# Optimization experiments

Measured on AMD Instinct MI355X. Metric: run time of the kernel, lower is better.

Reference implementation:

```python
import jax, jax.numpy as jnp
import numpy as np

B, NUM_PEAKS, PEAK_SIZE = 2, 64, 1000
MOTIF, HID, DEPTH, PROF_K = 640, 256, 7, 75


def conv1d(x, w, b, dilation=1):
    # x: (N, C, L), w: (O, I, K), valid padding
    out = jax.lax.conv_general_dilated(
        x, w, window_strides=(1,), padding='VALID',
        rhs_dilation=(dilation,), dimension_numbers=('NCH', 'OIH', 'NCH'))
    return out + b[None, :, None]


def setup_inputs() -> dict:
    key = jax.random.key(0)
    ks = jax.random.split(key, 10)
    L = NUM_PEAKS * PEAK_SIZE
    x = jax.random.normal(ks[0], (B, L, MOTIF), dtype=jnp.float32)
    peak_split = jnp.full((B * NUM_PEAKS,), PEAK_SIZE, dtype=jnp.int64) if jax.config.jax_enable_x64 else jnp.full((B * NUM_PEAKS,), PEAK_SIZE, dtype=jnp.int32)
    n_peaks = jnp.full((B,), NUM_PEAKS, dtype=jnp.int32)
    # parameters (kaiming-ish small init)
    w_proj = jax.random.normal(ks[1], (HID, MOTIF, 1), dtype=jnp.float32) / np.sqrt(MOTIF)
    b_proj = jnp.zeros((HID,), jnp.float32)
    w_dil = jax.random.normal(ks[2], (DEPTH, HID, HID, 3), dtype=jnp.float32) / np.sqrt(3 * HID)
    b_dil = jnp.zeros((DEPTH, HID), jnp.float32)
    w_prof = jax.random.normal(ks[3], (1, HID, PROF_K), dtype=jnp.float32) / np.sqrt(PROF_K * HID)
    b_prof = jnp.zeros((1,), jnp.float32)
    w_atpm = jax.random.normal(ks[4], (1, HID), dtype=jnp.float32) / np.sqrt(HID)
    b_atpm = jnp.zeros((1,), jnp.float32)
    return {
        'x': x, 'peak_split': peak_split, 'n_peaks': n_peaks, 'max_n_peaks': NUM_PEAKS,
        'w_proj': w_proj, 'b_proj': b_proj, 'w_dil': w_dil, 'b_dil': b_dil,
        'w_prof': w_prof, 'b_prof': b_prof, 'w_atpm': w_atpm, 'b_atpm': b_atpm,
    }


def reference(x, peak_split, n_peaks, max_n_peaks,
              w_proj, b_proj, w_dil, b_dil, w_prof, b_prof, w_atpm, b_atpm):
    # fast path: all samples have max_n_peaks uniform-size peaks
    batch, length, _ = x.shape
    num_peaks = int(np.asarray(n_peaks)[0])
    peak_size = length // num_peaks
    # 1x1 motif projection: (B, L, MOTIF) -> (B, HID, L)
    h = conv1d(jnp.transpose(x, (0, 2, 1)), w_proj, b_proj)
    # split into peaks: (B*num_peaks, HID, peak_size)
    h = jnp.transpose(h, (0, 2, 1)).reshape(batch * num_peaks, peak_size, HID)
    h = jnp.transpose(h, (0, 2, 1))
    # dilated conv tower with residual crop
    for i in range(DEPTH):
        dilation = 2 ** (i + 1)
        out = conv1d(h, w_dil[i], b_dil[i], dilation=dilation)
        crop = (h.shape[-1] - out.shape[-1]) // 2
        h = jax.nn.relu(out) + h[..., crop:-crop]
    peak_atpm = h.mean(axis=2)                      # (N, HID)
    peak_profile = conv1d(h, w_prof, b_prof)        # (N, 1, out_len)
    peak_atpm = jax.nn.softplus(peak_atpm @ w_atpm.T + b_atpm)
    peak_atpm = peak_atpm.reshape(batch, num_peaks, 1)
    peak_profile = jax.nn.softplus(peak_profile.reshape(batch, -1))
    return (peak_atpm, peak_profile)
```

## Files before the change

kernel.cpp:

```cpp
#include <hip/hip_runtime.h>
#include <hip/hip_bf16.h>
#include <math.h>

#define HID 256
#define MOTIF 640
#define PEAK 1000
#define NPEAKS 128
#define DEPTHN 7
#define PROFK 75
#define FINLEN 492
#define PROFLEN 418

typedef unsigned short u16;
typedef unsigned int u32;
typedef _Float16 f16x8 __attribute__((ext_vector_type(8)));
typedef float f32x16 __attribute__((ext_vector_type(16)));

__device__ __forceinline__ u16 f2h(float f) {
    _Float16 h = (_Float16)f; u16 b; __builtin_memcpy(&b, &h, 2); return b;
}
__device__ __forceinline__ float h2f(u16 b) {
    _Float16 h; __builtin_memcpy(&h, &b, 2); return (float)h;
}
__device__ __forceinline__ float hlo(u32 u) { return h2f((u16)(u & 0xffff)); }
__device__ __forceinline__ float hhi(u32 u) { return h2f((u16)(u >> 16)); }
__device__ __forceinline__ u32 pk2h(float a, float b) {
    return (u32)f2h(a) | ((u32)f2h(b) << 16);
}

__global__ __launch_bounds__(256) void conv_wdil1(const float* __restrict__ w,
                                                  u16* __restrict__ wf,
                                                  float* zp) {
    int i = blockIdx.x * 256 + threadIdx.x;
    if (zp && i < NPEAKS) zp[i] = 0.f;
    int cil = i & 15; int j = i >> 4;
    int c = j & 255; j >>= 8;
    int ci16 = j & 15; int k = j >> 4;
    wf[i] = f2h(w[((size_t)c * HID + ci16 * 16 + cil) * 3 + k]);
}

__global__ __launch_bounds__(256) void conv_wproj(const float* __restrict__ w,
                                                  u16* __restrict__ wf) {
    int i = blockIdx.x * 256 + threadIdx.x;
    if (i >= MOTIF * HID) return;
    int ml = i & 15;
    int c = (i >> 4) & 255;
    int m16 = i >> 12;
    wf[i] = f2h(w[(size_t)c * MOTIF + m16 * 16 + ml]);
}

template<int TAPS, int KCI, int DIL, bool SRCF32, bool RESID, bool ATPM>
__global__ __launch_bounds__(256, 3) void mfma_gemm(
    const void* __restrict__ src, int in_len, int in_stride,
    const u16* __restrict__ wf, const float* __restrict__ bias,
    u16* __restrict__ dst, int out_len,
    const float* __restrict__ watpm, float* part)
{
    constexpr int R = 128 + (TAPS - 1) * DIL;
    __shared__ __attribute__((aligned(16))) u16 Bs[8 * R * 8];
    __shared__ float aw[4];
    const int tid = threadIdx.x;
    const int wave = tid >> 6, lane = tid & 63;
    const int col = lane & 31, half = lane >> 5;
    const int cg = wave & 1, tg = wave >> 1;
    const int t0 = blockIdx.x * 128;
    const int c0 = blockIdx.y * 128;
    const int n  = blockIdx.z;

    const float* snf = (const float*)src + (size_t)n * in_len * in_stride;
    const u16*   snh = (const u16*)src + (size_t)n * in_len * in_stride;

    f32x16 acc[2][2];
    #pragma unroll
    for (int cs = 0; cs < 2; ++cs)
        #pragma unroll
        for (int ts = 0; ts < 2; ++ts)
            #pragma unroll
            for (int q = 0; q < 16; ++q) acc[cs][ts][q] = 0.f;

    for (int ci0 = 0; ci0 < KCI; ci0 += 64) {
        __syncthreads();
        for (int s = tid; s < R * 8; s += 256) {
            const int r = s >> 3, ch = s & 7;
            int g = t0 + r; if (g > in_len - 1) g = in_len - 1;
            u16* d = &Bs[(ch * R + r) * 8];
            if (SRCF32) {
                const float* p = snf + (size_t)g * in_stride + ci0 + ch * 8;
                float4 a = *(const float4*)p;
                float4 b = *(const float4*)(p + 4);
                uint4 o;
                o.x = pk2h(a.x, a.y); o.y = pk2h(a.z, a.w);
                o.z = pk2h(b.x, b.y); o.w = pk2h(b.z, b.w);
                *(uint4*)d = o;
            } else {
                *(uint4*)d = *(const uint4*)(snh + (size_t)g * in_stride + ci0 + ch * 8);
            }
        }
        __syncthreads();
        #pragma unroll
        for (int k = 0; k < TAPS; ++k) {
            #pragma unroll
            for (int s2 = 0; s2 < 4; ++s2) {
                const int ktile = k * (KCI / 16) + (ci0 >> 4) + s2;
                f16x8 bfv[2];
                #pragma unroll
                for (int ts = 0; ts < 2; ++ts)
                    bfv[ts] = *reinterpret_cast<const f16x8*>(
                        &Bs[((s2 * 2 + half) * R + tg * 64 + ts * 32 + col + k * DIL) * 8]);
                #pragma unroll
                for (int cs = 0; cs < 2; ++cs) {
                    const f16x8 af = *reinterpret_cast<const f16x8*>(
                        wf + ((size_t)(ktile * 256 + c0 + cg * 64 + cs * 32 + col) * 16 + half * 8));
                    acc[cs][0] = __builtin_amdgcn_mfma_f32_32x32x16_f16(af, bfv[0], acc[cs][0], 0, 0, 0);
                    acc[cs][1] = __builtin_amdgcn_mfma_f32_32x32x16_f16(af, bfv[1], acc[cs][1], 0, 0, 0);
                }
            }
        }
    }

    float apart = 0.f;
    #pragma unroll
    for (int ts = 0; ts < 2; ++ts) {
        const int t = t0 + tg * 64 + ts * 32 + col;
        if (t >= out_len) continue;
        const float* resf = snf + (size_t)(t + DIL) * in_stride;
        const u16*   resh = snh + (size_t)(t + DIL) * in_stride;
        u16* oh = dst + ((size_t)n * out_len + t) * HID;
        #pragma unroll
        for (int cs = 0; cs < 2; ++cs) {
            #pragma unroll
            for (int g = 0; g < 4; ++g) {
                const int c = c0 + cg * 64 + cs * 32 + g * 8 + half * 4;
                float4 bv = *(const float4*)(bias + c);
                float v0 = acc[cs][ts][g * 4 + 0] + bv.x;
                float v1 = acc[cs][ts][g * 4 + 1] + bv.y;
                float v2 = acc[cs][ts][g * 4 + 2] + bv.z;
                float v3 = acc[cs][ts][g * 4 + 3] + bv.w;
                if (RESID) {
                    if (SRCF32) {
                        float4 r = *(const float4*)(resf + c);
                        v0 = fmaxf(v0, 0.f) + r.x;
                        v1 = fmaxf(v1, 0.f) + r.y;
                        v2 = fmaxf(v2, 0.f) + r.z;
                        v3 = fmaxf(v3, 0.f) + r.w;
                    } else {
                        uint2 r = *(const uint2*)(resh + c);
                        v0 = fmaxf(v0, 0.f) + hlo(r.x);
                        v1 = fmaxf(v1, 0.f) + hhi(r.x);
                        v2 = fmaxf(v2, 0.f) + hlo(r.y);
                        v3 = fmaxf(v3, 0.f) + hhi(r.y);
                    }
                }
                if (ATPM) {
                    float4 wv = *(const float4*)(watpm + c);
                    apart += v0 * wv.x + v1 * wv.y + v2 * wv.z + v3 * wv.w;
                }
                uint2 o; o.x = pk2h(v0, v1); o.y = pk2h(v2, v3);
                *(uint2*)(oh + c) = o;
            }
        }
    }
    if (ATPM) {
        #pragma unroll
        for (int off = 32; off; off >>= 1) apart += __shfl_down(apart, off, 64);
        if (lane == 0) aw[wave] = apart;
        __syncthreads();
        if (tid == 0) atomicAdd(part + n, aw[0] + aw[1] + aw[2] + aw[3]);
    }
}

__global__ void atpm_fin(const float* __restrict__ part,
                         const float* __restrict__ batpm, float* __restrict__ out) {
    int i = threadIdx.x;
    float tot = part[i] / (float)FINLEN + batpm[0];
    out[i] = fmaxf(tot, 0.f) + log1pf(expf(-fabsf(tot)));
}

__global__ __launch_bounds__(256) void prof_kernel(
    const u16* __restrict__ h, const float* __restrict__ wprof,
    const float* __restrict__ bprof, float* __restrict__ out)
{
    __shared__ __attribute__((aligned(16))) float hs[64 * 204];
    __shared__ float red[128 * 8];
    const int tid = threadIdx.x;
    const int wave = tid >> 6, lane = tid & 63;
    const int ts = lane & 31, hw = lane >> 5;
    const int cig = wave * 2 + hw;
    const int n = blockIdx.y, t0 = blockIdx.x * 128;
    const u16* hn = h + (size_t)n * FINLEN * HID;
    float acc[4] = {0.f, 0.f, 0.f, 0.f};

    for (int ci0 = 0; ci0 < HID; ci0 += 64) {
        __syncthreads();
        {
            const int ci = tid & 63, rg = tid >> 6;
            for (int base = 0; base < 204; base += 16) {
                const int r0 = base + rg * 4;
                if (r0 >= 204) continue;
                float4 v;
                float* vp = (float*)&v;
                #pragma unroll
                for (int j = 0; j < 4; ++j) {
                    int g = t0 + r0 + j; if (g > FINLEN - 1) g = FINLEN - 1;
                    vp[j] = h2f(hn[(size_t)g * HID + ci0 + ci]);
                }
                *(float4*)&hs[ci * 204 + r0] = v;
            }
        }
        __syncthreads();
        for (int ci = 0; ci < 8; ++ci) {
            const int cia = cig * 8 + ci;
            const float4* hrow = (const float4*)&hs[cia * 204];
            const float* wrow = wprof + (size_t)(ci0 + cia) * PROFK;
            float wqf[84];
            #pragma unroll
            for (int q = 0; q < 3; ++q) wqf[q] = 0.f;
            #pragma unroll
            for (int q = 78; q < 84; ++q) wqf[q] = 0.f;
            #pragma unroll
            for (int k = 0; k < PROFK; ++k) wqf[k + 3] = wrow[k];
            #pragma unroll
            for (int m = 0; m < 20; ++m) {
                float4 h4 = hrow[ts + m];
                const float* hp = (const float*)&h4;
                #pragma unroll
                for (int j = 0; j < 4; ++j) {
                    #pragma unroll
                    for (int a = 0; a < 4; ++a) {
                        acc[a] += wqf[4 * m + j - a + 3] * hp[j];
                    }
                }
            }
        }
    }
    #pragma unroll
    for (int a = 0; a < 4; ++a) red[(ts * 4 + a) * 8 + cig] = acc[a];
    __syncthreads();
    if (tid < 128) {
        float s = 0.f;
        #pragma unroll
        for (int c8 = 0; c8 < 8; ++c8) s += red[tid * 8 + c8];
        const int t = t0 + tid;
        if (t < PROFLEN) {
            float v = s + bprof[0];
            out[(size_t)n * PROFLEN + t] = fmaxf(v, 0.f) + log1pf(expf(-fabsf(v)));
        }
    }
}

extern "C" void kernel_launch(void* const* d_in, const int* in_sizes, int n_in,
                              void* d_out, int out_size, void* d_ws, size_t ws_size,
                              hipStream_t stream) {
    const float* x     = (const float*)d_in[0];
    const float* wproj = (const float*)d_in[4];
    const float* bproj = (const float*)d_in[5];
    const float* wdil  = (const float*)d_in[6];
    const float* bdil  = (const float*)d_in[7];
    const float* wprof = (const float*)d_in[8];
    const float* bprof = (const float*)d_in[9];
    const float* watpm = (const float*)d_in[10];
    const float* batpm = (const float*)d_in[11];
    float* outAtpm = (float*)d_out;
    float* outProf = outAtpm + NPEAKS;

    char* ws = (char*)d_ws;
    u16* hA    = (u16*)ws;
    u16* hB    = (u16*)(ws + 65536000);
    u16* wpf   = (u16*)(ws + 131072000);
    u16* wslot = (u16*)(ws + 131399680);
    float* part = (float*)(ws + 131792896);

    conv_wproj<<<(MOTIF * HID + 255) / 256, 256, 0, stream>>>(wproj, wpf);

    mfma_gemm<1, MOTIF, 0, true, false, false><<<dim3(8, 2, NPEAKS), 256, 0, stream>>>(
        x, PEAK, MOTIF, wpf, bproj, hA, PEAK, nullptr, nullptr);

    #define LAYER(i, DIL, SRC, DST, INL, OUTL, TT)                                          \
        conv_wdil1<<<768, 256, 0, stream>>>(wdil + (size_t)(i) * HID * HID * 3, wslot,      \
                                            nullptr);                                       \
        mfma_gemm<3, HID, DIL, false, true, false><<<dim3(TT, 2, NPEAKS), 256, 0, stream>>>( \
            SRC, INL, HID, wslot, bdil + (size_t)(i) * HID, DST, OUTL, nullptr, nullptr);
    LAYER(0,   2, hA, hB, 1000, 996, 8)
    LAYER(1,   4, hB, hA,  996, 988, 8)
    LAYER(2,   8, hA, hB,  988, 972, 8)
    LAYER(3,  16, hB, hA,  972, 940, 8)
    LAYER(4,  32, hA, hB,  940, 876, 7)
    LAYER(5,  64, hB, hA,  876, 748, 6)
    #undef LAYER
    conv_wdil1<<<768, 256, 0, stream>>>(wdil + (size_t)6 * HID * HID * 3, wslot, part);
    mfma_gemm<3, HID, 128, false, true, true><<<dim3(4, 2, NPEAKS), 256, 0, stream>>>(
        hA, 748, HID, wslot, bdil + (size_t)6 * HID, hB, 492, watpm, part);

    atpm_fin<<<1, 128, 0, stream>>>(part, batpm, outAtpm);
    prof_kernel<<<dim3(4, NPEAKS), 256, 0, stream>>>(hB, wprof, bprof, outProf);
}
```

Measured before the change: 1.260 ms.

## Stage conv inputs via direct global-to-LDS loads with XOR swizzle, batch weight conversion

The dilated-conv GEMM now fills its shared-memory activation tile with global_load_lds 16-byte transfers, which bypass registers. The tile changes from a channel-major layout to a row-major one with an XOR swizzle on the 8-element slot, meant to avoid LDS bank conflicts on the MFMA operand reads. Weight conversion for all seven layers is merged into one launch writing separate slots, which removes six small kernel launches and the serialization between layers. The cost is a full vmcnt(0) wait before the barrier and a larger workspace footprint.

```diff
diff --git a/kernel.cpp b/kernel.cpp
--- a/kernel.cpp
+++ b/kernel.cpp
@@ -28,15 +28,24 @@
     return (u32)f2h(a) | ((u32)f2h(b) << 16);
 }
 
-__global__ __launch_bounds__(256) void conv_wdil1(const float* __restrict__ w,
-                                                  u16* __restrict__ wf,
-                                                  float* zp) {
+__device__ __forceinline__ void gll16(const void* g, void* l) {
+    __builtin_amdgcn_global_load_lds(
+        (const __attribute__((address_space(1))) void*)g,
+        (__attribute__((address_space(3))) void*)l, 16, 0, 0);
+}
+
+__global__ __launch_bounds__(256) void conv_wdil_all(const float* __restrict__ w,
+                                                     u16* __restrict__ wf,
+                                                     float* __restrict__ zp) {
+    const int layer = blockIdx.y;
     int i = blockIdx.x * 256 + threadIdx.x;
-    if (zp && i < NPEAKS) zp[i] = 0.f;
+    if (layer == 0 && i < NPEAKS) zp[i] = 0.f;
+    const float* wl = w + (size_t)layer * HID * HID * 3;
+    u16* wfl = wf + (size_t)layer * (3 * HID * HID);
     int cil = i & 15; int j = i >> 4;
     int c = j & 255; j >>= 8;
     int ci16 = j & 15; int k = j >> 4;
-    wf[i] = f2h(w[((size_t)c * HID + ci16 * 16 + cil) * 3 + k]);
+    wfl[i] = f2h(wl[((size_t)c * HID + ci16 * 16 + cil) * 3 + k]);
 }
 
 __global__ __launch_bounds__(256) void conv_wproj(const float* __restrict__ w,
@@ -57,7 +66,7 @@
     const float* __restrict__ watpm, float* part)
 {
     constexpr int R = 128 + (TAPS - 1) * DIL;
-    __shared__ __attribute__((aligned(16))) u16 Bs[8 * R * 8];
+    __shared__ __attribute__((aligned(16))) u16 Bs[R * 64];
     __shared__ float aw[4];
     const int tid = threadIdx.x;
     const int wave = tid >> 6, lane = tid & 63;
@@ -80,11 +89,11 @@
 
     for (int ci0 = 0; ci0 < KCI; ci0 += 64) {
         __syncthreads();
-        for (int s = tid; s < R * 8; s += 256) {
-            const int r = s >> 3, ch = s & 7;
-            int g = t0 + r; if (g > in_len - 1) g = in_len - 1;
-            u16* d = &Bs[(ch * R + r) * 8];
-            if (SRCF32) {
+        if (SRCF32) {
+            for (int s = tid; s < R * 8; s += 256) {
+                const int r = s >> 3, ch = s & 7;
+                int g = t0 + r; if (g > in_len - 1) g = in_len - 1;
+                u16* d = &Bs[(size_t)(((r << 3) + (ch ^ (r & 7))) << 3)];
                 const float* p = snf + (size_t)g * in_stride + ci0 + ch * 8;
                 float4 a = *(const float4*)p;
                 float4 b = *(const float4*)(p + 4);
@@ -92,9 +101,21 @@
                 o.x = pk2h(a.x, a.y); o.y = pk2h(a.z, a.w);
                 o.z = pk2h(b.x, b.y); o.w = pk2h(b.z, b.w);
                 *(uint4*)d = o;
-            } else {
-                *(uint4*)d = *(const uint4*)(snh + (size_t)g * in_stride + ci0 + ch * 8);
-            }
+            }
+        } else {
+            constexpr int ITERS = (R * 8 + 255) / 256;
+            #pragma unroll
+            for (int it = 0; it < ITERS; ++it) {
+                const int s = it * 256 + tid;
+                if (s < R * 8) {
+                    const int r = s >> 3, ch = s & 7;
+                    int g = t0 + r; if (g > in_len - 1) g = in_len - 1;
+                    const u16* gp = snh + (size_t)g * in_stride + ci0 + ((ch ^ (r & 7)) << 3);
+                    u16* lp = Bs + ((size_t)s << 3);
+                    gll16(gp, lp);
+                }
+            }
+            asm volatile("s_waitcnt vmcnt(0)" ::: "memory");
         }
         __syncthreads();
         #pragma unroll
@@ -104,9 +125,12 @@
                 const int ktile = k * (KCI / 16) + (ci0 >> 4) + s2;
                 f16x8 bfv[2];
                 #pragma unroll
-                for (int ts = 0; ts < 2; ++ts)
+                for (int ts = 0; ts < 2; ++ts) {
+                    const int row = tg * 64 + ts * 32 + col + k * DIL;
+                    const int slot = (s2 * 2 + half) ^ (row & 7);
                     bfv[ts] = *reinterpret_cast<const f16x8*>(
-                        &Bs[((s2 * 2 + half) * R + tg * 64 + ts * 32 + col + k * DIL) * 8]);
+                        &Bs[(size_t)(((row << 3) + slot) << 3)]);
+                }
                 #pragma unroll
                 for (int cs = 0; cs < 2; ++cs) {
                     const f16x8 af = *reinterpret_cast<const f16x8*>(
@@ -268,18 +292,18 @@
     u16* hB    = (u16*)(ws + 65536000);
     u16* wpf   = (u16*)(ws + 131072000);
     u16* wslot = (u16*)(ws + 131399680);
-    float* part = (float*)(ws + 131792896);
+    float* part = (float*)(ws + 134152192);
 
     conv_wproj<<<(MOTIF * HID + 255) / 256, 256, 0, stream>>>(wproj, wpf);
+    conv_wdil_all<<<dim3(768, DEPTHN), 256, 0, stream>>>(wdil, wslot, part);
 
     mfma_gemm<1, MOTIF, 0, true, false, false><<<dim3(8, 2, NPEAKS), 256, 0, stream>>>(
         x, PEAK, MOTIF, wpf, bproj, hA, PEAK, nullptr, nullptr);
 
-    #define LAYER(i, DIL, SRC, DST, INL, OUTL, TT)                                          \
-        conv_wdil1<<<768, 256, 0, stream>>>(wdil + (size_t)(i) * HID * HID * 3, wslot,      \
-                                            nullptr);                                       \
+    #define LAYER(i, DIL, SRC, DST, INL, OUTL, TT)                                           \
         mfma_gemm<3, HID, DIL, false, true, false><<<dim3(TT, 2, NPEAKS), 256, 0, stream>>>( \
-            SRC, INL, HID, wslot, bdil + (size_t)(i) * HID, DST, OUTL, nullptr, nullptr);
+            SRC, INL, HID, wslot + (size_t)(i) * (3 * HID * HID),                            \
+            bdil + (size_t)(i) * HID, DST, OUTL, nullptr, nullptr);
     LAYER(0,   2, hA, hB, 1000, 996, 8)
     LAYER(1,   4, hB, hA,  996, 988, 8)
     LAYER(2,   8, hA, hB,  988, 972, 8)
@@ -287,9 +311,9 @@
     LAYER(4,  32, hA, hB,  940, 876, 7)
     LAYER(5,  64, hB, hA,  876, 748, 6)
     #undef LAYER
-    conv_wdil1<<<768, 256, 0, stream>>>(wdil + (size_t)6 * HID * HID * 3, wslot, part);
     mfma_gemm<3, HID, 128, false, true, true><<<dim3(4, 2, NPEAKS), 256, 0, stream>>>(
-        hA, 748, HID, wslot, bdil + (size_t)6 * HID, hB, 492, watpm, part);
+        hA, 748, HID, wslot + (size_t)6 * (3 * HID * HID), bdil + (size_t)6 * HID,
+        hB, 492, watpm, part);
 
     atpm_fin<<<1, 128, 0, stream>>>(part, batpm, outAtpm);
     prof_kernel<<<dim3(4, NPEAKS), 256, 0, stream>>>(hB, wprof, bprof, outProf);
```

Measured after the change: 1.299 ms. +3.1%, slower.
